# Kernel optimization log

Hardware: AMD Instinct MI355X
Metric: run time of the kernel (lower is better)

Reference implementation:

```python
import jax, jax.numpy as jnp
import numpy as np

B, M, D, OUT = 16384, 4096, 512, 128


def setup_inputs() -> dict:
    key = jax.random.key(0)
    ks = jax.random.split(key, 5)
    x = jax.random.normal(ks[0], (B, D), dtype=jnp.float32)
    support = jax.random.normal(ks[1], (M, D), dtype=jnp.float32)
    gamma = jnp.float32(1.0)
    head_w = jax.random.normal(ks[2], (OUT, M), dtype=jnp.float32) / np.sqrt(M)
    head_b = jax.random.normal(ks[3], (OUT,), dtype=jnp.float32) * 0.01
    scale = jnp.ones((1,), dtype=jnp.float32)
    shift = jnp.zeros((1,), dtype=jnp.float32)
    return {"x": x, "support": support, "gamma": gamma,
            "head_w": head_w, "head_b": head_b,
            "scale": scale, "shift": shift}


def reference(x, support, gamma, head_w, head_b, scale, shift):
    x2 = jnp.sum(x * x, axis=-1, keepdims=True)           # [B, 1]
    s2 = jnp.sum(support * support, axis=-1)              # [M]
    xs = jnp.einsum('bd,md->bm', x, support)              # [B, M]
    sqdist = jnp.maximum(x2 + s2[None, :] - 2.0 * xs, 0.0)
    k = jnp.exp(-gamma * sqdist)                          # RBF kernel [B, M]
    out = jnp.einsum('bm,om->bo', k, head_w) + head_b     # linear head [B, OUT]
    return scale * out + shift
```

## Files before the change

### kernel.cpp

```cpp
#include <hip/hip_runtime.h>

typedef unsigned int u32;
typedef unsigned short u16;
typedef __attribute__((ext_vector_type(8))) __bf16 bf16x8;
typedef __attribute__((ext_vector_type(4))) float f32x4;

#define NB 16384
#define NM 4096
#define ND 512
#define NOUT 128
#define L2E 1.44269504088896340736f


__device__ __forceinline__ u16 f2bf(float f) {
  u32 u = __float_as_uint(f);
  u += 0x7FFFu + ((u >> 16) & 1u);
  return (u16)(u >> 16);
}

__device__ __forceinline__ void stage16(const u16* g, u16* l) {
  __builtin_amdgcn_global_load_lds((__attribute__((address_space(1))) void*)g,
                                   (__attribute__((address_space(3))) void*)l,
                                   16, 0, 0);
}

__device__ __forceinline__ uint4 pack8(float4 v0, float4 v1) {
  uint4 pk;
  pk.x = (u32)f2bf(v0.x) | ((u32)f2bf(v0.y) << 16);
  pk.y = (u32)f2bf(v0.z) | ((u32)f2bf(v0.w) << 16);
  pk.z = (u32)f2bf(v1.x) | ((u32)f2bf(v1.y) << 16);
  pk.w = (u32)f2bf(v1.z) | ((u32)f2bf(v1.w) << 16);
  return pk;
}

__global__ __launch_bounds__(256) void prep_all(const float* __restrict__ x,
                                                const float* __restrict__ s,
                                                const float* __restrict__ hw,
                                                const float* __restrict__ gamma_p,
                                                u16* __restrict__ x_ws,
                                                u16* __restrict__ s_ws,
                                                u16* __restrict__ hw_ws,
                                                float* __restrict__ x2g,
                                                float* __restrict__ s2g,
                                                float* __restrict__ out) {
  __shared__ uint4 t[2048];
  const int tid = threadIdx.x, bid = blockIdx.x;
  const int lane = tid & 63, w = tid >> 6;

  if (bid < 640) {
    const bool isx = bid < 512;
    const int blk = isx ? bid : (bid - 512);
    const float* src_m = isx ? x : s;
    u16* dst_ws        = isx ? x_ws : s_ws;
    float* sq_out      = isx ? x2g : s2g;
    const float gl   = gamma_p[0] * L2E;
    const float cmul = isx ? 1.0f : (-2.0f * gl);
    const int big = blk >> 2, roff = (blk & 3) * 32;

    #pragma unroll
    for (int p = 0; p < 8; ++p) {
      const int row = p * 4 + w;
      const float* src = src_m + (size_t)(blk * 32 + row) * ND + lane * 8;
      float4 v0 = *(const float4*)src;
      float4 v1 = *(const float4*)(src + 4);
      float ss = v0.x*v0.x + v0.y*v0.y + v0.z*v0.z + v0.w*v0.w
               + v1.x*v1.x + v1.y*v1.y + v1.z*v1.z + v1.w*v1.w;
      #pragma unroll
      for (int off = 32; off > 0; off >>= 1) ss += __shfl_down(ss, off);
      if (lane == 0) sq_out[blk * 32 + row] = gl * ss;
      v0.x *= cmul; v0.y *= cmul; v0.z *= cmul; v0.w *= cmul;
      v1.x *= cmul; v1.y *= cmul; v1.z *= cmul; v1.w *= cmul;
      t[lane * 32 + ((row + lane) & 31)] = pack8(v0, v1);
    }
    __syncthreads();
    #pragma unroll
    for (int p = 0; p < 8; ++p) {
      const int kg = p * 8 + (tid >> 5);
      const int row = tid & 31;
      uint4 pk = t[kg * 32 + ((row + kg) & 31)];
      *(uint4*)&dst_ws[(((size_t)(big * 64 + kg)) * 128 + roff + row) * 8] = pk;
    }
  } else if (bid < 672) {
    const int blk = bid - 640;
    #pragma unroll
    for (int p = 0; p < 8; ++p) {
      const int o = p * 16 + (tid >> 4);
      const int kg = tid & 15;
      const float* src = hw + (size_t)o * NM + blk * 128 + kg * 8;
      float4 v0 = *(const float4*)src;
      float4 v1 = *(const float4*)(src + 4);
      t[o * 16 + ((kg + o) & 15)] = pack8(v0, v1);
    }
    __syncthreads();
    #pragma unroll
    for (int it = 0; it < 8; ++it) {
      const int kg = it * 2 + (tid >> 7);
      const int o = tid & 127;
      uint4 pk = t[o * 16 + ((kg + o) & 15)];
      *(uint4*)&hw_ws[(((size_t)(blk * 16 + kg)) * 128 + o) * 8] = pk;
    }
  } else {
    float4* o4 = (float4*)out;
    const float4 z = {0.f, 0.f, 0.f, 0.f};
    size_t base = (size_t)(bid - 672) * 32768 + tid;
    #pragma unroll 8
    for (int i = 0; i < 128; ++i) o4[base + (size_t)i * 256] = z;
  }
}

__global__ __launch_bounds__(256, 2)
void rbf_fused(const u16* __restrict__ x_ws, const u16* __restrict__ s_ws,
               const u16* __restrict__ hw_ws, const float* __restrict__ x2g,
               const float* __restrict__ s2g, const float* __restrict__ head_b,
               const float* __restrict__ scale_p, const float* __restrict__ shift_p,
               float* __restrict__ out)
{
  __shared__ __align__(16) u16 smem[32768];

  const int tid  = threadIdx.x;
  const int w    = tid >> 6;
  const int lane = tid & 63;
  const int quad = lane >> 4;
  const int l16  = lane & 15;
  const int wr   = w & 1;
  const int wc   = w >> 1;
  const int xcd  = blockIdx.x & 7;
  const int rb   = (blockIdx.x >> 3) * 2 + (xcd & 1);
  const int half = xcd >> 1;
  const int b0   = rb * 128;

  const float vscale = scale_p[0];
  const float vshift = shift_p[0];

  const int sub  = w & 1;
  const int kgl0 = w >> 1;
  const int kgl1 = 2 + (w >> 1);
  const u16* xbase = x_ws + (size_t)rb * 65536 + (size_t)(sub * 64 + lane) * 8;
  const u16* sbase = s_ws + (size_t)(half * 8) * 65536 + (size_t)(sub * 64 + lane) * 8;
  const int dst0 = (kgl0 * 128 + sub * 64 + lane) * 8;
  const int dst1 = (kgl1 * 128 + sub * 64 + lane) * 8;

  f32x4 x2v[4];
  #pragma unroll
  for (int r = 0; r < 4; ++r)
    x2v[r] = *(const f32x4*)&x2g[b0 + wr * 64 + r * 16 + quad * 4];

  const f32x4 zf = {0.f, 0.f, 0.f, 0.f};
  f32x4 acc_xs[4][4];
  f32x4 acc_out[4][4];
  #pragma unroll
  for (int r = 0; r < 4; ++r)
    #pragma unroll
    for (int c = 0; c < 4; ++c) { acc_xs[r][c] = zf; acc_out[r][c] = zf; }

  auto stage_chunk = [&](int g) {
    const int kc  = g & 15;
    const int mt  = g >> 4;
    const int buf = g & 1;
    const u16* xs = xbase + (size_t)(kc * 4) * 1024;
    const u16* ss = sbase + (size_t)mt * 65536 + (size_t)(kc * 4) * 1024;
    stage16(xs + kgl0 * 1024, &smem[buf * 4096 + dst0]);
    stage16(xs + kgl1 * 1024, &smem[buf * 4096 + dst1]);
    stage16(ss + kgl0 * 1024, &smem[8192 + buf * 4096 + dst0]);
    stage16(ss + kgl1 * 1024, &smem[8192 + buf * 4096 + dst1]);
  };

  auto compute_chunk = [&](int buf) {
    bf16x8 av[4], bv[4];
    #pragma unroll
    for (int r = 0; r < 4; ++r)
      av[r] = *(const bf16x8*)&smem[buf * 4096 + (quad * 128 + wr * 64 + r * 16 + l16) * 8];
    #pragma unroll
    for (int c = 0; c < 4; ++c)
      bv[c] = *(const bf16x8*)&smem[8192 + buf * 4096 + (quad * 128 + wc * 64 + c * 16 + l16) * 8];
    #pragma unroll
    for (int r = 0; r < 4; ++r)
      #pragma unroll
      for (int c = 0; c < 4; ++c)
        acc_xs[r][c] = __builtin_amdgcn_mfma_f32_16x16x32_bf16(av[r], bv[c], acc_xs[r][c], 0, 0, 0);
  };

  auto gemm2_step = [&](int mtg2, int ks) {
    const int kg = ks * 4 + quad;
    bf16x8 a2[4], b2[4];
    #pragma unroll
    for (int r = 0; r < 4; ++r)
      a2[r] = *(const bf16x8*)&smem[16384 + kg * 1024 + (wr * 64 + r * 16 + l16) * 8];
    const size_t slab = (size_t)(mtg2 * 16 + kg);
    #pragma unroll
    for (int c = 0; c < 4; ++c)
      b2[c] = *(const bf16x8*)(hw_ws + (slab * 128 + wc * 64 + c * 16 + l16) * 8);
    #pragma unroll
    for (int r = 0; r < 4; ++r)
      #pragma unroll
      for (int c = 0; c < 4; ++c)
        acc_out[r][c] = __builtin_amdgcn_mfma_f32_16x16x32_bf16(a2[r], b2[c], acc_out[r][c], 0, 0, 0);
  };

  stage_chunk(0);
  __syncthreads();

  #pragma unroll 1
  for (int mt = 0; mt < 8; ++mt) {
    const int mtg = half * 8 + mt;
    #pragma unroll 2
    for (int kc = 0; kc < 16; ++kc) {
      const int g = (mt << 4) | kc;
      if (g + 1 < 128) stage_chunk(g + 1);
      compute_chunk(g & 1);
      if (mt > 0 && (kc & 3) == 0) gemm2_step(mtg - 1, kc >> 2);
      if (kc < 15) __syncthreads();
    }

    {
      float s2v[4];
      #pragma unroll
      for (int c = 0; c < 4; ++c)
        s2v[c] = s2g[mtg * 128 + wc * 64 + c * 16 + l16];
      #pragma unroll
      for (int r = 0; r < 4; ++r)
        #pragma unroll
        for (int c = 0; c < 4; ++c) {
          const int cl = wc * 64 + c * 16 + l16;
          const int kbase = 16384 + (cl >> 3) * 1024 + (cl & 7);
          #pragma unroll
          for (int i = 0; i < 4; ++i) {
            const int row = wr * 64 + r * 16 + quad * 4 + i;
            const float t = acc_xs[r][c][i] + x2v[r][i] + s2v[c];
            float kv = __builtin_amdgcn_exp2f(-t);
            kv = fminf(kv, 1.0f);
            smem[kbase + row * 8] = (u16)(__float_as_uint(kv) >> 16);
            acc_xs[r][c][i] = 0.0f;
          }
        }
    }
    __syncthreads();
  }

  #pragma unroll
  for (int ks = 0; ks < 4; ++ks)
    gemm2_step(half * 8 + 7, ks);

  float addv[4];
  #pragma unroll
  for (int c = 0; c < 4; ++c) {
    const int col = wc * 64 + c * 16 + l16;
    addv[c] = (half == 0) ? (vscale * head_b[col] + vshift) : 0.0f;
  }
  #pragma unroll
  for (int r = 0; r < 4; ++r)
    #pragma unroll
    for (int c = 0; c < 4; ++c) {
      const int col = wc * 64 + c * 16 + l16;
      #pragma unroll
      for (int i = 0; i < 4; ++i) {
        const int row = b0 + wr * 64 + r * 16 + quad * 4 + i;
        atomicAdd(&out[(size_t)row * NOUT + col], vscale * acc_out[r][c][i] + addv[c]);
      }
    }
}

extern "C" void kernel_launch(void* const* d_in, const int* in_sizes, int n_in,
                              void* d_out, int out_size, void* d_ws, size_t ws_size,
                              hipStream_t stream) {
  const float* x       = (const float*)d_in[0];
  const float* support = (const float*)d_in[1];
  const float* gamma   = (const float*)d_in[2];
  const float* head_w  = (const float*)d_in[3];
  const float* head_b  = (const float*)d_in[4];
  const float* scale   = (const float*)d_in[5];
  const float* shift   = (const float*)d_in[6];
  float* out = (float*)d_out;

  char* w = (char*)d_ws;
  u16*   x_ws  = (u16*)(w);
  u16*   s_ws  = (u16*)(w + 16777216);
  u16*   hw_ws = (u16*)(w + 20971520);
  float* x2g   = (float*)(w + 22020096);
  float* s2g   = (float*)(w + 22085632);

  prep_all<<<688, 256, 0, stream>>>(x, support, head_w, gamma,
                                    x_ws, s_ws, hw_ws, x2g, s2g, out);
  rbf_fused<<<512, 256, 0, stream>>>(x_ws, s_ws, hw_ws, x2g, s2g,
                                     head_b, scale, shift, out);
}
```

Measured before the change: 206.4 us.

## Use FP8 MFMA for the distance GEMM and halve the row tile per block

Measured after the change: 198.2 us. -4.0%, faster.

```diff
diff --git a/kernel.cpp b/kernel.cpp
--- a/kernel.cpp
+++ b/kernel.cpp
@@ -2,6 +2,7 @@
 
 typedef unsigned int u32;
 typedef unsigned short u16;
+typedef unsigned char u8;
 typedef __attribute__((ext_vector_type(8))) __bf16 bf16x8;
 typedef __attribute__((ext_vector_type(4))) float f32x4;
 
@@ -18,13 +19,24 @@
   return (u16)(u >> 16);
 }
 
-__device__ __forceinline__ void stage16(const u16* g, u16* l) {
+__device__ __forceinline__ u8 f2fp8(float f) {
+  u32 u = __float_as_uint(f);
+  u32 s = (u >> 24) & 0x80u;
+  u32 au = u & 0x7FFFFFFFu;
+  if (au < 0x3C800000u) return (u8)s;
+  au += 0x000FFFFFu + ((au >> 20) & 1u);
+  u32 e = (au >> 23) - 120u;
+  u32 m = (au >> 20) & 7u;
+  return (u8)(s | (e << 3) | m);
+}
+
+__device__ __forceinline__ void stage16(const void* g, void* l) {
   __builtin_amdgcn_global_load_lds((__attribute__((address_space(1))) void*)g,
                                    (__attribute__((address_space(3))) void*)l,
                                    16, 0, 0);
 }
 
-__device__ __forceinline__ uint4 pack8(float4 v0, float4 v1) {
+__device__ __forceinline__ uint4 pack8bf(float4 v0, float4 v1) {
   uint4 pk;
   pk.x = (u32)f2bf(v0.x) | ((u32)f2bf(v0.y) << 16);
   pk.y = (u32)f2bf(v0.z) | ((u32)f2bf(v0.w) << 16);
@@ -33,17 +45,27 @@
   return pk;
 }
 
+__device__ __forceinline__ uint2 pack8f8(float4 v0, float4 v1) {
+  uint2 pk;
+  pk.x = (u32)f2fp8(v0.x) | ((u32)f2fp8(v0.y) << 8) |
+         ((u32)f2fp8(v0.z) << 16) | ((u32)f2fp8(v0.w) << 24);
+  pk.y = (u32)f2fp8(v1.x) | ((u32)f2fp8(v1.y) << 8) |
+         ((u32)f2fp8(v1.z) << 16) | ((u32)f2fp8(v1.w) << 24);
+  return pk;
+}
+
 __global__ __launch_bounds__(256) void prep_all(const float* __restrict__ x,
                                                 const float* __restrict__ s,
                                                 const float* __restrict__ hw,
                                                 const float* __restrict__ gamma_p,
-                                                u16* __restrict__ x_ws,
-                                                u16* __restrict__ s_ws,
+                                                u8*  __restrict__ x_ws,
+                                                u8*  __restrict__ s_ws,
                                                 u16* __restrict__ hw_ws,
                                                 float* __restrict__ x2g,
                                                 float* __restrict__ s2g,
                                                 float* __restrict__ out) {
-  __shared__ uint4 t[2048];
+  __shared__ uint2 t8[2048];
+  __shared__ uint4 t16[2048];
   const int tid = threadIdx.x, bid = blockIdx.x;
   const int lane = tid & 63, w = tid >> 6;
 
@@ -51,11 +73,13 @@
     const bool isx = bid < 512;
     const int blk = isx ? bid : (bid - 512);
     const float* src_m = isx ? x : s;
-    u16* dst_ws        = isx ? x_ws : s_ws;
-    float* sq_out      = isx ? x2g : s2g;
+    u8*    dst_ws = isx ? x_ws : s_ws;
+    float* sq_out = isx ? x2g : s2g;
     const float gl   = gamma_p[0] * L2E;
     const float cmul = isx ? 1.0f : (-2.0f * gl);
-    const int big = blk >> 2, roff = (blk & 3) * 32;
+    const int big  = isx ? (blk >> 1) : (blk >> 2);
+    const int roff = isx ? ((blk & 1) * 32) : ((blk & 3) * 32);
+    const int rows = isx ? 64 : 128;
 
     #pragma unroll
     for (int p = 0; p < 8; ++p) {
@@ -70,15 +94,15 @@
       if (lane == 0) sq_out[blk * 32 + row] = gl * ss;
       v0.x *= cmul; v0.y *= cmul; v0.z *= cmul; v0.w *= cmul;
       v1.x *= cmul; v1.y *= cmul; v1.z *= cmul; v1.w *= cmul;
-      t[lane * 32 + ((row + lane) & 31)] = pack8(v0, v1);
+      t8[lane * 32 + ((row + lane) & 31)] = pack8f8(v0, v1);
     }
     __syncthreads();
     #pragma unroll
     for (int p = 0; p < 8; ++p) {
       const int kg = p * 8 + (tid >> 5);
       const int row = tid & 31;
-      uint4 pk = t[kg * 32 + ((row + kg) & 31)];
-      *(uint4*)&dst_ws[(((size_t)(big * 64 + kg)) * 128 + roff + row) * 8] = pk;
+      uint2 pk = t8[kg * 32 + ((row + kg) & 31)];
+      *(uint2*)&dst_ws[(((size_t)(big * 64 + kg)) * rows + roff + row) * 8] = pk;
     }
   } else if (bid < 672) {
     const int blk = bid - 640;
@@ -89,14 +113,14 @@
       const float* src = hw + (size_t)o * NM + blk * 128 + kg * 8;
       float4 v0 = *(const float4*)src;
       float4 v1 = *(const float4*)(src + 4);
-      t[o * 16 + ((kg + o) & 15)] = pack8(v0, v1);
+      t16[o * 16 + ((kg + o) & 15)] = pack8bf(v0, v1);
     }
     __syncthreads();
     #pragma unroll
     for (int it = 0; it < 8; ++it) {
       const int kg = it * 2 + (tid >> 7);
       const int o = tid & 127;
-      uint4 pk = t[o * 16 + ((kg + o) & 15)];
+      uint4 pk = t16[o * 16 + ((kg + o) & 15)];
       *(uint4*)&hw_ws[(((size_t)(blk * 16 + kg)) * 128 + o) * 8] = pk;
     }
   } else {
@@ -109,13 +133,13 @@
 }
 
 __global__ __launch_bounds__(256, 2)
-void rbf_fused(const u16* __restrict__ x_ws, const u16* __restrict__ s_ws,
+void rbf_fused(const u8* __restrict__ x_ws, const u8* __restrict__ s_ws,
                const u16* __restrict__ hw_ws, const float* __restrict__ x2g,
                const float* __restrict__ s2g, const float* __restrict__ head_b,
                const float* __restrict__ scale_p, const float* __restrict__ shift_p,
                float* __restrict__ out)
 {
-  __shared__ __align__(16) u16 smem[32768];
+  __shared__ __align__(16) char smem[65536];
 
   const int tid  = threadIdx.x;
   const int w    = tid >> 6;
@@ -127,89 +151,85 @@
   const int xcd  = blockIdx.x & 7;
   const int rb   = (blockIdx.x >> 3) * 2 + (xcd & 1);
   const int half = xcd >> 1;
-  const int b0   = rb * 128;
+  const int b0   = rb * 64;
 
   const float vscale = scale_p[0];
   const float vshift = shift_p[0];
 
-  const int sub  = w & 1;
-  const int kgl0 = w >> 1;
-  const int kgl1 = 2 + (w >> 1);
-  const u16* xbase = x_ws + (size_t)rb * 65536 + (size_t)(sub * 64 + lane) * 8;
-  const u16* sbase = s_ws + (size_t)(half * 8) * 65536 + (size_t)(sub * 64 + lane) * 8;
-  const int dst0 = (kgl0 * 128 + sub * 64 + lane) * 8;
-  const int dst1 = (kgl1 * 128 + sub * 64 + lane) * 8;
-
-  f32x4 x2v[4];
-  #pragma unroll
-  for (int r = 0; r < 4; ++r)
-    x2v[r] = *(const f32x4*)&x2g[b0 + wr * 64 + r * 16 + quad * 4];
+  const u8* xsrc = x_ws + (size_t)rb * 32768;
+  const u8* ssrc = s_ws + (size_t)(half * 8) * 65536;
+
+  #pragma unroll
+  for (int i = 0; i < 8; ++i)
+    stage16(xsrc + i * 4096 + tid * 16, smem + i * 4096 + tid * 16);
+
+  f32x4 x2v[2];
+  #pragma unroll
+  for (int r = 0; r < 2; ++r)
+    x2v[r] = *(const f32x4*)&x2g[b0 + wr * 32 + r * 16 + quad * 4];
 
   const f32x4 zf = {0.f, 0.f, 0.f, 0.f};
-  f32x4 acc_xs[4][4];
-  f32x4 acc_out[4][4];
-  #pragma unroll
-  for (int r = 0; r < 4; ++r)
+  f32x4 acc_xs[2][4];
+  f32x4 acc_out[2][4];
+  #pragma unroll
+  for (int r = 0; r < 2; ++r)
     #pragma unroll
     for (int c = 0; c < 4; ++c) { acc_xs[r][c] = zf; acc_out[r][c] = zf; }
 
-  auto stage_chunk = [&](int g) {
-    const int kc  = g & 15;
-    const int mt  = g >> 4;
-    const int buf = g & 1;
-    const u16* xs = xbase + (size_t)(kc * 4) * 1024;
-    const u16* ss = sbase + (size_t)mt * 65536 + (size_t)(kc * 4) * 1024;
-    stage16(xs + kgl0 * 1024, &smem[buf * 4096 + dst0]);
-    stage16(xs + kgl1 * 1024, &smem[buf * 4096 + dst1]);
-    stage16(ss + kgl0 * 1024, &smem[8192 + buf * 4096 + dst0]);
-    stage16(ss + kgl1 * 1024, &smem[8192 + buf * 4096 + dst1]);
+  auto stage_sgrp = [&](int mt, int grp, int buf) {
+    const u8* sp = ssrc + (size_t)mt * 65536 + grp * 8192;
+    char* dp = smem + 32768 + buf * 8192;
+    stage16(sp + tid * 16, dp + tid * 16);
+    stage16(sp + 4096 + tid * 16, dp + 4096 + tid * 16);
   };
 
-  auto compute_chunk = [&](int buf) {
-    bf16x8 av[4], bv[4];
-    #pragma unroll
-    for (int r = 0; r < 4; ++r)
-      av[r] = *(const bf16x8*)&smem[buf * 4096 + (quad * 128 + wr * 64 + r * 16 + l16) * 8];
+  auto compute_kc = [&](int kc, int kcL, int buf) {
+    long long a[2], b[4];
+    #pragma unroll
+    for (int r = 0; r < 2; ++r)
+      a[r] = *(const long long*)(smem + ((kc * 4 + quad) * 64 + wr * 32 + r * 16 + l16) * 8);
     #pragma unroll
     for (int c = 0; c < 4; ++c)
-      bv[c] = *(const bf16x8*)&smem[8192 + buf * 4096 + (quad * 128 + wc * 64 + c * 16 + l16) * 8];
-    #pragma unroll
-    for (int r = 0; r < 4; ++r)
+      b[c] = *(const long long*)(smem + 32768 + buf * 8192 +
+                                 ((kcL * 4 + quad) * 128 + wc * 64 + c * 16 + l16) * 8);
+    #pragma unroll
+    for (int r = 0; r < 2; ++r)
       #pragma unroll
       for (int c = 0; c < 4; ++c)
-        acc_xs[r][c] = __builtin_amdgcn_mfma_f32_16x16x32_bf16(av[r], bv[c], acc_xs[r][c], 0, 0, 0);
+        acc_xs[r][c] = __builtin_amdgcn_mfma_f32_16x16x32_fp8_fp8(a[r], b[c], acc_xs[r][c], 0, 0, 0);
   };
 
   auto gemm2_step = [&](int mtg2, int ks) {
     const int kg = ks * 4 + quad;
-    bf16x8 a2[4], b2[4];
-    #pragma unroll
-    for (int r = 0; r < 4; ++r)
-      a2[r] = *(const bf16x8*)&smem[16384 + kg * 1024 + (wr * 64 + r * 16 + l16) * 8];
+    bf16x8 a2[2], b2[4];
+    #pragma unroll
+    for (int r = 0; r < 2; ++r)
+      a2[r] = *(const bf16x8*)(smem + 49152 + (kg * 64 + wr * 32 + r * 16 + l16) * 16);
     const size_t slab = (size_t)(mtg2 * 16 + kg);
     #pragma unroll
     for (int c = 0; c < 4; ++c)
       b2[c] = *(const bf16x8*)(hw_ws + (slab * 128 + wc * 64 + c * 16 + l16) * 8);
     #pragma unroll
-    for (int r = 0; r < 4; ++r)
+    for (int r = 0; r < 2; ++r)
       #pragma unroll
       for (int c = 0; c < 4; ++c)
         acc_out[r][c] = __builtin_amdgcn_mfma_f32_16x16x32_bf16(a2[r], b2[c], acc_out[r][c], 0, 0, 0);
   };
 
-  stage_chunk(0);
+  stage_sgrp(0, 0, 0);
   __syncthreads();
 
   #pragma unroll 1
   for (int mt = 0; mt < 8; ++mt) {
     const int mtg = half * 8 + mt;
-    #pragma unroll 2
-    for (int kc = 0; kc < 16; ++kc) {
-      const int g = (mt << 4) | kc;
-      if (g + 1 < 128) stage_chunk(g + 1);
-      compute_chunk(g & 1);
-      if (mt > 0 && (kc & 3) == 0) gemm2_step(mtg - 1, kc >> 2);
-      if (kc < 15) __syncthreads();
+    #pragma unroll
+    for (int grp = 0; grp < 8; ++grp) {
+      if (grp < 7)      stage_sgrp(mt, grp + 1, (grp + 1) & 1);
+      else if (mt < 7)  stage_sgrp(mt + 1, 0, 0);
+      compute_kc(grp * 2,     0, grp & 1);
+      compute_kc(grp * 2 + 1, 1, grp & 1);
+      if (mt > 0 && (grp & 1) == 0) gemm2_step(mtg - 1, grp >> 1);
+      if (grp < 7) __syncthreads();
     }
 
     {
@@ -218,18 +238,18 @@
       for (int c = 0; c < 4; ++c)
         s2v[c] = s2g[mtg * 128 + wc * 64 + c * 16 + l16];
       #pragma unroll
-      for (int r = 0; r < 4; ++r)
+      for (int r = 0; r < 2; ++r)
         #pragma unroll
         for (int c = 0; c < 4; ++c) {
           const int cl = wc * 64 + c * 16 + l16;
-          const int kbase = 16384 + (cl >> 3) * 1024 + (cl & 7);
+          char* kbase = smem + 49152 + (cl >> 3) * 1024 + (cl & 7) * 2;
           #pragma unroll
           for (int i = 0; i < 4; ++i) {
-            const int row = wr * 64 + r * 16 + quad * 4 + i;
+            const int row = wr * 32 + r * 16 + quad * 4 + i;
             const float t = acc_xs[r][c][i] + x2v[r][i] + s2v[c];
             float kv = __builtin_amdgcn_exp2f(-t);
             kv = fminf(kv, 1.0f);
-            smem[kbase + row * 8] = (u16)(__float_as_uint(kv) >> 16);
+            *(u16*)(kbase + row * 16) = (u16)(__float_as_uint(kv) >> 16);
             acc_xs[r][c][i] = 0.0f;
           }
         }
@@ -248,13 +268,13 @@
     addv[c] = (half == 0) ? (vscale * head_b[col] + vshift) : 0.0f;
   }
   #pragma unroll
-  for (int r = 0; r < 4; ++r)
+  for (int r = 0; r < 2; ++r)
     #pragma unroll
     for (int c = 0; c < 4; ++c) {
       const int col = wc * 64 + c * 16 + l16;
       #pragma unroll
       for (int i = 0; i < 4; ++i) {
-        const int row = b0 + wr * 64 + r * 16 + quad * 4 + i;
+        const int row = b0 + wr * 32 + r * 16 + quad * 4 + i;
         atomicAdd(&out[(size_t)row * NOUT + col], vscale * acc_out[r][c][i] + addv[c]);
       }
     }
@@ -273,14 +293,14 @@
   float* out = (float*)d_out;
 
   char* w = (char*)d_ws;
-  u16*   x_ws  = (u16*)(w);
-  u16*   s_ws  = (u16*)(w + 16777216);
-  u16*   hw_ws = (u16*)(w + 20971520);
-  float* x2g   = (float*)(w + 22020096);
-  float* s2g   = (float*)(w + 22085632);
+  u8*    x_ws  = (u8*)(w);
+  u8*    s_ws  = (u8*)(w + 8388608);
+  u16*   hw_ws = (u16*)(w + 10485760);
+  float* x2g   = (float*)(w + 11534336);
+  float* s2g   = (float*)(w + 11599872);
 
   prep_all<<<688, 256, 0, stream>>>(x, support, head_w, gamma,
                                     x_ws, s_ws, hw_ws, x2g, s2g, out);
-  rbf_fused<<<512, 256, 0, stream>>>(x_ws, s_ws, hw_ws, x2g, s2g,
-                                     head_b, scale, shift, out);
-}
+  rbf_fused<<<1024, 256, 0, stream>>>(x_ws, s_ws, hw_ws, x2g, s2g,
+                                      head_b, scale, shift, out);
+}
```
